# Optimization experiments

Measured on AMD Instinct MI355X. Metric: run time of the kernel, lower is better.

Reference implementation:

```python
import jax, jax.numpy as jnp
import numpy as np

HIDDEN = 1024
ATTN = 512


def setup_inputs() -> dict:
    key = jax.random.key(0)
    ks = jax.random.split(key, 7)
    B, S = 8, 2048
    inputs = jax.random.normal(ks[0], (B, S, HIDDEN), dtype=jnp.float32)
    s = 1.0 / np.sqrt(HIDDEN)
    Wq = jax.random.uniform(ks[1], (HIDDEN, ATTN), jnp.float32, -s, s)
    bq = jax.random.uniform(ks[2], (ATTN,), jnp.float32, -s, s)
    Wk = jax.random.uniform(ks[3], (HIDDEN, ATTN), jnp.float32, -s, s)
    bk = jax.random.uniform(ks[4], (ATTN,), jnp.float32, -s, s)
    Wv = jax.random.uniform(ks[5], (HIDDEN, ATTN), jnp.float32, -s, s)
    bv = jax.random.uniform(ks[6], (ATTN,), jnp.float32, -s, s)
    return {"inputs": inputs, "Wq": Wq, "bq": bq, "Wk": Wk, "bk": bk, "Wv": Wv, "bv": bv}


def reference(inputs, Wq, bq, Wk, bk, Wv, bv):
    # tanh-gated Q/K/V projections
    q = jnp.tanh(inputs @ Wq + bq)        # [B, S, A]
    k = jnp.tanh(inputs @ Wk + bk)        # [B, S, A]
    v = jnp.tanh(inputs @ Wv + bv)        # [B, S, A]
    scores = jnp.einsum('bqa,bka->bqk', q, k) / jnp.sqrt(jnp.float32(ATTN))
    probs = jax.nn.softmax(scores, axis=-1)   # [B, S, S]
    context = jnp.einsum('bqk,bka->bqa', probs, v)
    return jnp.tanh(context), probs
```

## Files before the change

### kernel.cpp

```cpp
#include <hip/hip_runtime.h>
#include <hip/hip_fp16.h>
#include <cstdint>

#define HIDDEN 1024
#define ATTN   512
#define NB     8
#define SEQ    2048
#define MROWS  (NB*SEQ)

typedef _Float16 f16x8 __attribute__((ext_vector_type(8)));
typedef _Float16 f16x4 __attribute__((ext_vector_type(4)));
typedef float    f32x4 __attribute__((ext_vector_type(4)));


__device__ __forceinline__ float tanh_fast(float x){
  float e = __expf(2.0f*x);
  return 1.0f - 2.0f/(e + 1.0f);
}

__device__ __forceinline__ void gload16(const void* g, void* l){
  __builtin_amdgcn_global_load_lds((const __attribute__((address_space(1))) void*)g,
                                   (__attribute__((address_space(3))) void*)l, 16, 0, 0);
}

__global__ __launch_bounds__(256) void k_cast_x(const float* __restrict__ x, __half* __restrict__ xh){
  size_t i = (size_t)blockIdx.x*256 + threadIdx.x;
  const float4* src = reinterpret_cast<const float4*>(x) + i*2;
  float4 a = src[0], b = src[1];
  f16x8 h;
  h[0]=(_Float16)a.x; h[1]=(_Float16)a.y; h[2]=(_Float16)a.z; h[3]=(_Float16)a.w;
  h[4]=(_Float16)b.x; h[5]=(_Float16)b.y; h[6]=(_Float16)b.z; h[7]=(_Float16)b.w;
  reinterpret_cast<f16x8*>(xh)[i] = h;
}

__global__ __launch_bounds__(256) void k_transpose_w(const float* __restrict__ Wq, const float* __restrict__ Wk,
                                                     const float* __restrict__ Wv, __half* __restrict__ whT){
  __shared__ float lds[32][33];
  int which = blockIdx.y;
  const float* W = which==0 ? Wq : (which==1 ? Wk : Wv);
  int tr = blockIdx.x >> 4;
  int tc = blockIdx.x & 15;
  int t = threadIdx.x;
  {
    int r = t >> 3, c4 = (t & 7)*4;
    float4 v = *reinterpret_cast<const float4*>(W + (size_t)(tr*32 + r)*ATTN + tc*32 + c4);
    lds[r][c4+0]=v.x; lds[r][c4+1]=v.y; lds[r][c4+2]=v.z; lds[r][c4+3]=v.w;
  }
  __syncthreads();
  {
    int n = t >> 3, k4 = (t & 7)*4;
    ushort4 u;
    u.x = __half_as_ushort(__float2half(lds[k4+0][n]));
    u.y = __half_as_ushort(__float2half(lds[k4+1][n]));
    u.z = __half_as_ushort(__float2half(lds[k4+2][n]));
    u.w = __half_as_ushort(__float2half(lds[k4+3][n]));
    *reinterpret_cast<ushort4*>(whT + (size_t)which*ATTN*HIDDEN + (size_t)(tc*32 + n)*HIDDEN + tr*32 + k4) = u;
  }
}

__global__ __launch_bounds__(256,3) void k_proj(const __half* __restrict__ xh, const __half* __restrict__ whT,
                                                const float* __restrict__ bq, const float* __restrict__ bk,
                                                const float* __restrict__ bv,
                                                __half* __restrict__ qh, __half* __restrict__ kh, __half* __restrict__ vT){
  __shared__ __align__(16) _Float16 lA[128*64];
  __shared__ __align__(16) _Float16 lB[128*64];
  int nt = blockIdx.x;
  int m0 = blockIdx.y * 128;
  int which = nt >> 2;
  int ncol0 = (nt & 3) * 128;
  int t = threadIdx.x;
  int w = t >> 6, lane = t & 63;
  int lrow = lane & 15, lk = lane >> 4;
  int wm = w >> 1, wn = w & 1;

  int rr = lane >> 3;
  int ss = (lane & 7) ^ rr;
  const __half* Abase = xh + (size_t)(m0 + w*32 + rr)*HIDDEN + ss*8;
  const __half* Bbase = whT + (size_t)which*ATTN*HIDDEN + (size_t)(ncol0 + w*32 + rr)*HIDDEN + ss*8;
  _Float16* lAw = &lA[(w*32)*64];
  _Float16* lBw = &lB[(w*32)*64];

  f32x4 acc[4][4];
  #pragma unroll
  for (int i=0;i<4;i++)
    #pragma unroll
    for (int j=0;j<4;j++) acc[i][j] = f32x4{0.f,0.f,0.f,0.f};

  for (int k0 = 0; k0 < HIDDEN; k0 += 64){
    __syncthreads();
    #pragma unroll
    for (int c=0; c<4; c++){
      gload16(Abase + (size_t)c*8*HIDDEN + k0, &lAw[c*8*64]);
      gload16(Bbase + (size_t)c*8*HIDDEN + k0, &lBw[c*8*64]);
    }
    __syncthreads();
    #pragma unroll
    for (int u=0; u<2; u++){
      f16x8 af[4], bf[4];
      #pragma unroll
      for (int fm=0; fm<4; fm++){
        int row = wm*64 + fm*16 + lrow;
        af[fm] = *(const f16x8*)&lA[row*64 + (((u*4 + lk) ^ (row & 7))*8)];
      }
      #pragma unroll
      for (int fn=0; fn<4; fn++){
        int row = wn*64 + fn*16 + lrow;
        bf[fn] = *(const f16x8*)&lB[row*64 + (((u*4 + lk) ^ (row & 7))*8)];
      }
      #pragma unroll
      for (int fm=0; fm<4; fm++)
        #pragma unroll
        for (int fn=0; fn<4; fn++)
          acc[fm][fn] = __builtin_amdgcn_mfma_f32_16x16x32_f16(af[fm], bf[fn], acc[fm][fn], 0,0,0);
    }
  }

  const float* bias = which==0 ? bq : (which==1 ? bk : bv);
  if (which < 2){
    __half* dst = which==0 ? qh : kh;
    int rt_base = (m0 >> 4) + wm*4;
    int at_base = (ncol0 >> 5) + wn*2;
    #pragma unroll
    for (int fn=0; fn<4; fn++){
      int col = ncol0 + wn*64 + fn*16 + lrow;
      float bb = bias[col];
      int at = at_base + (fn >> 1);
      int asub = (fn & 1)*16 + lrow;
      #pragma unroll
      for (int fm=0; fm<4; fm++){
        size_t tbase = (size_t)(rt_base + fm)*8192 + (size_t)at*512 + asub;
        #pragma unroll
        for (int mi=0; mi<4; mi++)
          dst[tbase + (lk*4 + mi)*32] = __float2half(tanh_fast(acc[fm][fn][mi] + bb));
      }
    }
  } else {
    __half* vb = vT + (size_t)(m0 >> 11)*ATTN*SEQ;
    int jb0 = (m0 & 2047) + wm*64;
    int at0 = (ncol0 >> 4) + wn*4;
    #pragma unroll
    for (int fn=0; fn<4; fn++){
      int col = ncol0 + wn*64 + fn*16 + lrow;
      float bb = bias[col];
      #pragma unroll
      for (int fm=0; fm<4; fm++){
        int jb = jb0 + fm*16;
        f16x4 h;
        #pragma unroll
        for (int mi=0; mi<4; mi++) h[mi] = (_Float16)tanh_fast(acc[fm][fn][mi] + bb);
        *(f16x4*)(vb + (size_t)(at0 + fn)*32768 + (size_t)(jb >> 5)*512 + lrow*32 + (jb & 16) + lk*4) = h;
      }
    }
  }
}

__global__ __launch_bounds__(1024,4) void k_scores(const __half* __restrict__ qh, const __half* __restrict__ kh,
                                                   float* __restrict__ probs, __half* __restrict__ p16){
  __shared__ float red[16][32];
  int bid = blockIdx.x;
  int b  = bid & 7;
  int i0 = (bid >> 3) * 32;
  int t = threadIdx.x;
  int w = t >> 6, lane = t & 63;
  int lrow = lane & 15, lk = lane >> 4;
  int loff = lrow*32 + lk*8;

  const __half* kbase = kh + (size_t)((b*SEQ + w*128) >> 4)*8192 + loff;
  const __half* qbase = qh + (size_t)((b*SEQ + i0) >> 4)*8192 + loff;

  f32x4 acc[2][8];
  #pragma unroll
  for (int i=0;i<2;i++)
    #pragma unroll
    for (int j=0;j<8;j++) acc[i][j] = f32x4{0.f,0.f,0.f,0.f};

  for (int it = 0; it < 16; it++){
    f16x8 aq0 = *(const f16x8*)(qbase + it*512);
    f16x8 aq1 = *(const f16x8*)(qbase + 8192 + it*512);
    #pragma unroll
    for (int fn=0; fn<8; fn++){
      f16x8 kf = *(const f16x8*)(kbase + (size_t)fn*8192 + it*512);
      acc[0][fn] = __builtin_amdgcn_mfma_f32_16x16x32_f16(kf, aq0, acc[0][fn], 0,0,0);
      acc[1][fn] = __builtin_amdgcn_mfma_f32_16x16x32_f16(kf, aq1, acc[1][fn], 0,0,0);
    }
  }

  const float scale = 0.044194173824159216f;
  float sm[2];
  #pragma unroll
  for (int nf=0;nf<2;nf++){
    float s = 0.f;
    #pragma unroll
    for (int fn=0;fn<8;fn++)
      #pragma unroll
      for (int mi=0;mi<4;mi++){
        float e = __expf(acc[nf][fn][mi] * scale);
        acc[nf][fn][mi] = e;
        s += e;
      }
    s += __shfl_xor(s, 16);
    s += __shfl_xor(s, 32);
    sm[nf] = s;
  }
  if (lane < 16){ red[w][lane] = sm[0]; red[w][16 + lane] = sm[1]; }
  __syncthreads();
  float inv[2];
  #pragma unroll
  for (int nf=0;nf<2;nf++){
    float tot = 0.f;
    #pragma unroll
    for (int ww=0; ww<16; ww++) tot += red[ww][nf*16 + lrow];
    inv[nf] = 1.0f / tot;
  }
  #pragma unroll
  for (int nf=0;nf<2;nf++){
    f32x4 iv = {inv[nf], inv[nf], inv[nf], inv[nf]};
    size_t tq = (size_t)((i0 >> 4) + nf);
    #pragma unroll
    for (int fn=0;fn<8;fn++){
      f32x4 v = acc[nf][fn] * iv;
      if (probs){
        size_t rowoff = (size_t)(i0 + nf*16 + lrow)*SEQ + w*128 + lk*4;
        *(f32x4*)(probs + (size_t)b*SEQ*SEQ + rowoff + fn*16) = v;
      }
      if (p16){
        f16x4 h;
        h[0]=(_Float16)v[0]; h[1]=(_Float16)v[1]; h[2]=(_Float16)v[2]; h[3]=(_Float16)v[3];
        *(f16x4*)&p16[(size_t)b*SEQ*SEQ + tq*32768 + (size_t)(w*4 + (fn>>1))*512 + lrow*32 + (fn&1)*16 + lk*4] = h;
      }
    }
  }
}

__global__ __launch_bounds__(512,4) void k_pv_p16(const __half* __restrict__ p16, const __half* __restrict__ vT,
                                                  float* __restrict__ probs, float* __restrict__ out0){
  int bid = blockIdx.x;
  int b  = bid & 7;
  int i0 = (bid >> 3) * 64;
  int t = threadIdx.x;
  int w = t >> 6, lane = t & 63;
  int lrow = lane & 15, lk = lane >> 4;
  int loff = lrow*32 + lk*8;

  const __half* pbase = p16 + (size_t)b*SEQ*SEQ + (size_t)(i0 >> 4)*32768 + loff;
  const __half* vbase = vT + (size_t)b*ATTN*SEQ + (size_t)(w*4)*32768 + loff;
  float* prow = probs + ((size_t)b*SEQ + i0 + lrow)*SEQ + lk*8;

  f32x4 acc[4][4];
  #pragma unroll
  for (int i=0;i<4;i++)
    #pragma unroll
    for (int j=0;j<4;j++) acc[i][j] = f32x4{0.f,0.f,0.f,0.f};

  for (int kt = 0; kt < 64; kt++){
    f16x8 pa[4];
    #pragma unroll
    for (int nf=0; nf<4; nf++)
      pa[nf] = *(const f16x8*)(pbase + (size_t)nf*32768 + kt*512);
    if ((kt >> 3) == w){
      #pragma unroll
      for (int nf=0; nf<4; nf++){
        f32x4 lo = {(float)pa[nf][0], (float)pa[nf][1], (float)pa[nf][2], (float)pa[nf][3]};
        f32x4 hi = {(float)pa[nf][4], (float)pa[nf][5], (float)pa[nf][6], (float)pa[nf][7]};
        float* pr = prow + (size_t)nf*16*SEQ + kt*32;
        __builtin_nontemporal_store(lo, (f32x4*)(pr));
        __builtin_nontemporal_store(hi, (f32x4*)(pr + 4));
      }
    }
    #pragma unroll
    for (int cf=0; cf<4; cf++){
      f16x8 bv8 = *(const f16x8*)(vbase + (size_t)cf*32768 + kt*512);
      #pragma unroll
      for (int nf=0; nf<4; nf++)
        acc[nf][cf] = __builtin_amdgcn_mfma_f32_16x16x32_f16(pa[nf], bv8, acc[nf][cf], 0,0,0);
    }
  }

  float* dst = out0 + ((size_t)b*SEQ + i0)*ATTN + w*64;
  #pragma unroll
  for (int nf=0; nf<4; nf++)
    #pragma unroll
    for (int cf=0; cf<4; cf++)
      #pragma unroll
      for (int mi=0; mi<4; mi++)
        __builtin_nontemporal_store(tanh_fast(acc[nf][cf][mi]),
                                    dst + (size_t)(nf*16 + lk*4 + mi)*ATTN + cf*16 + lrow);
}

__global__ __launch_bounds__(512,4) void k_pv(const float* __restrict__ probs, const __half* __restrict__ vT,
                                              float* __restrict__ out0){
  int bid = blockIdx.x;
  int b  = bid & 7;
  int i0 = (bid >> 3) * 32;
  int t = threadIdx.x;
  int w = t >> 6, lane = t & 63;
  int lrow = lane & 15, lk = lane >> 4;
  int loff = lrow*32 + lk*8;

  const float* pbase = probs + ((size_t)b*SEQ + i0 + lrow)*SEQ + lk*8;
  const __half* vbase = vT + (size_t)b*ATTN*SEQ + (size_t)(w*4)*32768 + loff;

  f32x4 acc[2][4];
  #pragma unroll
  for (int i=0;i<2;i++)
    #pragma unroll
    for (int j=0;j<4;j++) acc[i][j] = f32x4{0.f,0.f,0.f,0.f};

  for (int kt = 0; kt < 64; kt++){
    int k0 = kt*32;
    f16x8 af[2];
    #pragma unroll
    for (int nf=0; nf<2; nf++){
      const float* pr = pbase + (size_t)nf*16*SEQ + k0;
      float4 a = *(const float4*)(pr);
      float4 c = *(const float4*)(pr + 4);
      f16x8 h;
      h[0]=(_Float16)a.x; h[1]=(_Float16)a.y; h[2]=(_Float16)a.z; h[3]=(_Float16)a.w;
      h[4]=(_Float16)c.x; h[5]=(_Float16)c.y; h[6]=(_Float16)c.z; h[7]=(_Float16)c.w;
      af[nf] = h;
    }
    #pragma unroll
    for (int cf=0; cf<4; cf++){
      f16x8 bv8 = *(const f16x8*)(vbase + (size_t)cf*32768 + kt*512);
      acc[0][cf] = __builtin_amdgcn_mfma_f32_16x16x32_f16(af[0], bv8, acc[0][cf], 0,0,0);
      acc[1][cf] = __builtin_amdgcn_mfma_f32_16x16x32_f16(af[1], bv8, acc[1][cf], 0,0,0);
    }
  }

  float* dst = out0 + ((size_t)b*SEQ + i0)*ATTN + w*64;
  #pragma unroll
  for (int nf=0; nf<2; nf++)
    #pragma unroll
    for (int cf=0; cf<4; cf++)
      #pragma unroll
      for (int mi=0; mi<4; mi++)
        dst[(size_t)(nf*16 + lk*4 + mi)*ATTN + cf*16 + lrow] = tanh_fast(acc[nf][cf][mi]);
}

extern "C" void kernel_launch(void* const* d_in, const int* in_sizes, int n_in,
                              void* d_out, int out_size, void* d_ws, size_t ws_size,
                              hipStream_t stream){
  const float* x  = (const float*)d_in[0];
  const float* Wq = (const float*)d_in[1];
  const float* bq = (const float*)d_in[2];
  const float* Wk = (const float*)d_in[3];
  const float* bk = (const float*)d_in[4];
  const float* Wv = (const float*)d_in[5];
  const float* bv = (const float*)d_in[6];

  float* out0 = (float*)d_out;
  float* out1 = out0 + (size_t)NB*SEQ*ATTN;

  const size_t SZ = 16777216;
  char* ws = (char*)d_ws;

  if (ws_size >= 5*SZ){
    __half* vT  = (__half*)ws;
    __half* p16 = (__half*)(ws + SZ);
    __half* xh  = (__half*)out1;
    __half* whT = (__half*)((char*)out1 + 2*SZ);
    __half* qh  = (__half*)((char*)out1 + 2*SZ + 3145728);
    __half* kh  = (__half*)((char*)out1 + 3*SZ + 3145728);
    k_cast_x     <<<8192,        256, 0, stream>>>(x, xh);
    k_transpose_w<<<dim3(512,3), 256, 0, stream>>>(Wq, Wk, Wv, whT);
    k_proj       <<<dim3(12,128),256, 0, stream>>>(xh, whT, bq, bk, bv, qh, kh, vT);
    k_scores     <<<512,        1024, 0, stream>>>(qh, kh, (float*)nullptr, p16);
    k_pv_p16     <<<256,         512, 0, stream>>>(p16, vT, out1, out0);
  } else if (ws_size >= 3*SZ){
    __half* vT = (__half*)ws;
    __half* qh = (__half*)(ws + SZ);
    __half* kh = (__half*)(ws + 2*SZ);
    __half* xh  = (__half*)out1;
    __half* whT = (__half*)((char*)out1 + 2*SZ);
    k_cast_x     <<<8192,        256, 0, stream>>>(x, xh);
    k_transpose_w<<<dim3(512,3), 256, 0, stream>>>(Wq, Wk, Wv, whT);
    k_proj       <<<dim3(12,128),256, 0, stream>>>(xh, whT, bq, bk, bv, qh, kh, vT);
    k_scores     <<<512,        1024, 0, stream>>>(qh, kh, out1, ((__half*)nullptr));
    k_pv         <<<512,         512, 0, stream>>>(out1, vT, out0);
  } else {
    __half* vT = (__half*)ws;
    __half* qh = (__half*)out0;
    __half* kh = (__half*)out0 + (size_t)MROWS*ATTN;
    __half* xh  = (__half*)out1;
    __half* whT = (__half*)((char*)out1 + 2*SZ);
    k_cast_x     <<<8192,        256, 0, stream>>>(x, xh);
    k_transpose_w<<<dim3(512,3), 256, 0, stream>>>(Wq, Wk, Wv, whT);
    k_proj       <<<dim3(12,128),256, 0, stream>>>(xh, whT, bq, bk, bv, qh, kh, vT);
    k_scores     <<<512,        1024, 0, stream>>>(qh, kh, out1, ((__half*)nullptr));
    k_pv         <<<512,         512, 0, stream>>>(out1, vT, out0);
  }
}
```

Measured before the change: 278.1 us.

## Defer softmax normalization to PV kernel and compute unnormalized exp scores

Adds a new scores kernel that writes exp(qk*scale) in fp16 without row-max subtraction or row-sum reduction. It stages Q and K tiles into LDS via direct global-to-LDS loads. Row sums are accumulated in the PV kernel, which normalizes both the context output and the fp32 probs it writes. This removes the cross-wave reduction and sync from the scores stage. Skipping the max subtraction is safe only because tanh bounds q and k, and the probs write now re-reads p16 after the main loop.

```diff
diff --git a/kernel.cpp b/kernel.cpp
--- a/kernel.cpp
+++ b/kernel.cpp
@@ -154,8 +154,71 @@
   }
 }
 
+__global__ __launch_bounds__(512,2) void k_scoresE(const __half* __restrict__ qh, const __half* __restrict__ kh,
+                                                   __half* __restrict__ p16){
+  __shared__ __align__(16) _Float16 qlds[4*16*512];
+  __shared__ __align__(16) _Float16 khlds[32*512];
+  int bid = blockIdx.x;
+  int b  = bid & 7;
+  int i0 = (bid >> 3) * 64;
+  int t = threadIdx.x;
+  int w = t >> 6, lane = t & 63;
+  int lrow = lane & 15, lk = lane >> 4;
+
+  const __half* qsrc = qh + (size_t)((b*SEQ + i0) >> 4)*8192;
+  const __half* ksrc = kh + (size_t)b*SEQ*ATTN;
+  __half* pb = p16 + (size_t)b*SEQ*SEQ;
+
+  #pragma unroll
+  for (int r=0; r<8; r++){
+    int chunk = r*8 + w;
+    gload16(qsrc + (size_t)chunk*512 + lane*8, &qlds[chunk*512]);
+  }
+
+  const float scale = 0.044194173824159216f;
+  for (int ko = 0; ko < 4; ko++){
+    f32x4 acc[4][4];
+    #pragma unroll
+    for (int i=0;i<4;i++)
+      #pragma unroll
+      for (int j=0;j<4;j++) acc[i][j] = f32x4{0.f,0.f,0.f,0.f};
+
+    for (int it = 0; it < 16; it++){
+      __syncthreads();
+      #pragma unroll
+      for (int j=0; j<4; j++){
+        int c = w*4 + j;
+        gload16(ksrc + (size_t)(ko*32 + c)*8192 + it*512 + lane*8, &khlds[c*512]);
+      }
+      __syncthreads();
+      f16x8 kf[4], qf[4];
+      #pragma unroll
+      for (int j=0;j<4;j++) kf[j] = *(const f16x8*)&khlds[(w*4+j)*512 + lrow*32 + lk*8];
+      #pragma unroll
+      for (int j=0;j<4;j++) qf[j] = *(const f16x8*)&qlds[(j*16 + it)*512 + lrow*32 + lk*8];
+      #pragma unroll
+      for (int fn=0; fn<4; fn++)
+        #pragma unroll
+        for (int qi=0; qi<4; qi++)
+          acc[qi][fn] = __builtin_amdgcn_mfma_f32_16x16x32_f16(kf[fn], qf[qi], acc[qi][fn], 0,0,0);
+    }
+
+    #pragma unroll
+    for (int qi=0; qi<4; qi++){
+      size_t tq = (size_t)((i0 >> 4) + qi)*32768;
+      #pragma unroll
+      for (int fn=0; fn<4; fn++){
+        f16x4 h;
+        #pragma unroll
+        for (int mi=0; mi<4; mi++) h[mi] = (_Float16)__expf(acc[qi][fn][mi]*scale);
+        *(f16x4*)&pb[tq + (size_t)(ko*16 + w*2 + (fn>>1))*512 + lrow*32 + (fn&1)*16 + lk*4] = h;
+      }
+    }
+  }
+}
+
 __global__ __launch_bounds__(1024,4) void k_scores(const __half* __restrict__ qh, const __half* __restrict__ kh,
-                                                   float* __restrict__ probs, __half* __restrict__ p16){
+                                                   float* __restrict__ probs){
   __shared__ float red[16][32];
   int bid = blockIdx.x;
   int b  = bid & 7;
@@ -215,25 +278,19 @@
   #pragma unroll
   for (int nf=0;nf<2;nf++){
     f32x4 iv = {inv[nf], inv[nf], inv[nf], inv[nf]};
-    size_t tq = (size_t)((i0 >> 4) + nf);
     #pragma unroll
     for (int fn=0;fn<8;fn++){
       f32x4 v = acc[nf][fn] * iv;
-      if (probs){
-        size_t rowoff = (size_t)(i0 + nf*16 + lrow)*SEQ + w*128 + lk*4;
-        *(f32x4*)(probs + (size_t)b*SEQ*SEQ + rowoff + fn*16) = v;
-      }
-      if (p16){
-        f16x4 h;
-        h[0]=(_Float16)v[0]; h[1]=(_Float16)v[1]; h[2]=(_Float16)v[2]; h[3]=(_Float16)v[3];
-        *(f16x4*)&p16[(size_t)b*SEQ*SEQ + tq*32768 + (size_t)(w*4 + (fn>>1))*512 + lrow*32 + (fn&1)*16 + lk*4] = h;
-      }
+      size_t rowoff = (size_t)(i0 + nf*16 + lrow)*SEQ + w*128 + lk*4;
+      *(f32x4*)(probs + (size_t)b*SEQ*SEQ + rowoff + fn*16) = v;
     }
   }
 }
 
 __global__ __launch_bounds__(512,4) void k_pv_p16(const __half* __restrict__ p16, const __half* __restrict__ vT,
                                                   float* __restrict__ probs, float* __restrict__ out0){
+  __shared__ float partial[8][64];
+  __shared__ float rsum[64];
   int bid = blockIdx.x;
   int b  = bid & 7;
   int i0 = (bid >> 3) * 64;
@@ -244,13 +301,13 @@
 
   const __half* pbase = p16 + (size_t)b*SEQ*SEQ + (size_t)(i0 >> 4)*32768 + loff;
   const __half* vbase = vT + (size_t)b*ATTN*SEQ + (size_t)(w*4)*32768 + loff;
-  float* prow = probs + ((size_t)b*SEQ + i0 + lrow)*SEQ + lk*8;
 
   f32x4 acc[4][4];
   #pragma unroll
   for (int i=0;i<4;i++)
     #pragma unroll
     for (int j=0;j<4;j++) acc[i][j] = f32x4{0.f,0.f,0.f,0.f};
+  float esum[4] = {0.f,0.f,0.f,0.f};
 
   for (int kt = 0; kt < 64; kt++){
     f16x8 pa[4];
@@ -260,11 +317,10 @@
     if ((kt >> 3) == w){
       #pragma unroll
       for (int nf=0; nf<4; nf++){
-        f32x4 lo = {(float)pa[nf][0], (float)pa[nf][1], (float)pa[nf][2], (float)pa[nf][3]};
-        f32x4 hi = {(float)pa[nf][4], (float)pa[nf][5], (float)pa[nf][6], (float)pa[nf][7]};
-        float* pr = prow + (size_t)nf*16*SEQ + kt*32;
-        __builtin_nontemporal_store(lo, (f32x4*)(pr));
-        __builtin_nontemporal_store(hi, (f32x4*)(pr + 4));
+        float s = 0.f;
+        #pragma unroll
+        for (int j=0; j<8; j++) s += (float)pa[nf][j];
+        esum[nf] += s;
       }
     }
     #pragma unroll
@@ -276,15 +332,51 @@
     }
   }
 
+  #pragma unroll
+  for (int nf=0; nf<4; nf++){
+    esum[nf] += __shfl_xor(esum[nf], 16);
+    esum[nf] += __shfl_xor(esum[nf], 32);
+  }
+  if (lane < 16){
+    #pragma unroll
+    for (int nf=0; nf<4; nf++) partial[w][nf*16 + lane] = esum[nf];
+  }
+  __syncthreads();
+  if (t < 64){
+    float s = 0.f;
+    #pragma unroll
+    for (int ww=0; ww<8; ww++) s += partial[ww][t];
+    rsum[t] = s;
+  }
+  __syncthreads();
+
   float* dst = out0 + ((size_t)b*SEQ + i0)*ATTN + w*64;
   #pragma unroll
   for (int nf=0; nf<4; nf++)
     #pragma unroll
-    for (int cf=0; cf<4; cf++)
-      #pragma unroll
-      for (int mi=0; mi<4; mi++)
-        __builtin_nontemporal_store(tanh_fast(acc[nf][cf][mi]),
+    for (int mi=0; mi<4; mi++){
+      float iv = 1.0f / rsum[nf*16 + lk*4 + mi];
+      #pragma unroll
+      for (int cf=0; cf<4; cf++)
+        __builtin_nontemporal_store(tanh_fast(acc[nf][cf][mi]*iv),
                                     dst + (size_t)(nf*16 + lk*4 + mi)*ATTN + cf*16 + lrow);
+    }
+
+  float* prow = probs + ((size_t)b*SEQ + i0 + lrow)*SEQ + lk*8;
+  #pragma unroll
+  for (int nf=0; nf<4; nf++){
+    float iv = 1.0f / rsum[nf*16 + lrow];
+    #pragma unroll
+    for (int k2=0; k2<8; k2++){
+      int kt = w*8 + k2;
+      f16x8 pa = *(const f16x8*)(pbase + (size_t)nf*32768 + kt*512);
+      f32x4 lo = {(float)pa[0]*iv, (float)pa[1]*iv, (float)pa[2]*iv, (float)pa[3]*iv};
+      f32x4 hi = {(float)pa[4]*iv, (float)pa[5]*iv, (float)pa[6]*iv, (float)pa[7]*iv};
+      float* pr = prow + (size_t)nf*16*SEQ + kt*32;
+      __builtin_nontemporal_store(lo, (f32x4*)(pr));
+      __builtin_nontemporal_store(hi, (f32x4*)(pr + 4));
+    }
+  }
 }
 
 __global__ __launch_bounds__(512,4) void k_pv(const float* __restrict__ probs, const __half* __restrict__ vT,
@@ -364,7 +456,7 @@
     k_cast_x     <<<8192,        256, 0, stream>>>(x, xh);
     k_transpose_w<<<dim3(512,3), 256, 0, stream>>>(Wq, Wk, Wv, whT);
     k_proj       <<<dim3(12,128),256, 0, stream>>>(xh, whT, bq, bk, bv, qh, kh, vT);
-    k_scores     <<<512,        1024, 0, stream>>>(qh, kh, (float*)nullptr, p16);
+    k_scoresE    <<<256,         512, 0, stream>>>(qh, kh, p16);
     k_pv_p16     <<<256,         512, 0, stream>>>(p16, vT, out1, out0);
   } else if (ws_size >= 3*SZ){
     __half* vT = (__half*)ws;
@@ -375,7 +467,7 @@
     k_cast_x     <<<8192,        256, 0, stream>>>(x, xh);
     k_transpose_w<<<dim3(512,3), 256, 0, stream>>>(Wq, Wk, Wv, whT);
     k_proj       <<<dim3(12,128),256, 0, stream>>>(xh, whT, bq, bk, bv, qh, kh, vT);
-    k_scores     <<<512,        1024, 0, stream>>>(qh, kh, out1, ((__half*)nullptr));
+    k_scores     <<<512,        1024, 0, stream>>>(qh, kh, out1);
     k_pv         <<<512,         512, 0, stream>>>(out1, vT, out0);
   } else {
     __half* vT = (__half*)ws;
@@ -386,7 +478,7 @@
     k_cast_x     <<<8192,        256, 0, stream>>>(x, xh);
     k_transpose_w<<<dim3(512,3), 256, 0, stream>>>(Wq, Wk, Wv, whT);
     k_proj       <<<dim3(12,128),256, 0, stream>>>(xh, whT, bq, bk, bv, qh, kh, vT);
-    k_scores     <<<512,        1024, 0, stream>>>(qh, kh, out1, ((__half*)nullptr));
+    k_scores     <<<512,        1024, 0, stream>>>(qh, kh, out1);
     k_pv         <<<512,         512, 0, stream>>>(out1, vT, out0);
   }
 }
```

Measured after the change: 282.2 us. Within noise of the previous version (+1.5%).
